# Kernel optimization log

Measured on AMD Instinct MI355X. Metric: run time of the kernel, lower is better.

Reference implementation:

```python
import jax, jax.numpy as jnp
import numpy as np

ALPHA = 0.2          # LeakyReLU negative slope
NEG_INF = -9.0e15    # padding value used by the torch code before softmax


def setup_inputs() -> dict:
    key = jax.random.key(0)
    k1, k2, k3, k4 = jax.random.split(key, 4)
    B, N, F_IN, F_OUT = 32, 1024, 128, 128
    # Dense 0/1 adjacency with self-loops (every node has degree >= 1)
    u = jax.random.uniform(k1, (B, N, N))
    adj = (u < 0.03).astype(jnp.float32)
    adj = jnp.maximum(adj, jnp.eye(N, dtype=jnp.float32)[None, :, :])
    batch_features = jax.random.normal(k2, (B, N, F_IN), dtype=jnp.float32)
    W = jax.random.normal(k3, (F_OUT, F_IN), dtype=jnp.float32) * 0.1  # nn.Linear weight [out,in]
    a = jax.random.normal(k4, (2 * F_OUT, 1), dtype=jnp.float32) * 0.1
    return {"batch_graphs": adj, "batch_features": batch_features, "W": W, "a": a}


def reference(batch_graphs, batch_features, W, a):
    # batch_graphs: [B,N,N] 0/1 adjacency; batch_features: [B,N,F_in]
    D = W.shape[0]
    h = jnp.einsum('bnf,df->bnd', batch_features, W)  # fc (no bias), dropout=0 is a no-op
    # score(i,j) = LeakyReLU(a[:D].h_i + a[D:].h_j); concat order is [center_i || neighbor_j]
    a_src = a[:D, 0]
    a_dst = a[D:, 0]
    s = h @ a_src                                   # [B,N] center term
    t = h @ a_dst                                   # [B,N] neighbor term
    scores = s[:, :, None] + t[:, None, :]          # [B,N,N]
    scores = jnp.where(scores > 0, scores, ALPHA * scores)
    # segmented softmax over each node's neighbors (pad_sequence with -9e15 == masked softmax)
    masked = jnp.where(batch_graphs == 1.0, scores, NEG_INF)
    attn = jax.nn.softmax(masked, axis=-1) * batch_graphs  # *adj zeros non-edges exactly (and deg-0 rows)
    # weighted sum of neighbor features scattered back to each node
    out = jnp.einsum('bij,bjd->bid', attn, h)       # [B,N,D]
    return out
```

## Files before the change

kernel.cpp:

```cpp
#include <hip/hip_runtime.h>
#include <hip/hip_bf16.h>

#define B_ 32
#define N_ 1024
#define F_ 128
#define ALPHA_ 0.2f
#define PSTR 72

typedef __attribute__((ext_vector_type(8))) short short8_t;
typedef __attribute__((ext_vector_type(4))) short short4_t;
typedef __attribute__((ext_vector_type(4))) float f32x4;

static __device__ __forceinline__ unsigned short bf16b(float f) {
    return __bfloat16_as_ushort(__float2bfloat16(f));
}

__global__ __launch_bounds__(256) void hst_kernel(
    const float* __restrict__ feat, const float* __restrict__ W,
    const float* __restrict__ a, float* __restrict__ h,
    float* __restrict__ s_out, float* __restrict__ t_out)
{
    __shared__ unsigned short Wt[128 * 128];
    __shared__ float fl[64 * 128];
    const int tid = threadIdx.x;
    const long row0 = (long)blockIdx.x * 64;

    for (int i = tid; i < 128 * 128; i += 256) {
        int d = i >> 7, k = i & 127;
        Wt[k * 128 + d] = bf16b(W[i]);
    }
    for (int i = tid; i < 64 * 128; i += 256) {
        int r = i >> 7, k = i & 127;
        fl[r * 128 + ((k + 8 * (r >> 2)) & 127)] = feat[(row0 + r) * 128 + k];
    }
    __syncthreads();

    const int oct = tid & 15;
    const int rg  = tid >> 4;
    const int d0  = oct * 8;
    const int r0  = rg * 4;

    float acc[4][8];
    #pragma unroll
    for (int q = 0; q < 4; ++q)
        #pragma unroll
        for (int c = 0; c < 8; ++c) acc[q][c] = 0.f;

    for (int kc = 0; kc < 128; kc += 4) {
        float wv[4][8];
        #pragma unroll
        for (int kk = 0; kk < 4; ++kk) {
            short8_t wr = *reinterpret_cast<const short8_t*>(&Wt[(kc + kk) * 128 + d0]);
            #pragma unroll
            for (int c = 0; c < 8; ++c) {
                union { unsigned u; float f; } cv;
                cv.u = ((unsigned)(unsigned short)wr[c]) << 16;
                wv[kk][c] = cv.f;
            }
        }
        #pragma unroll
        for (int q = 0; q < 4; ++q) {
            int r = r0 + q;
            int koff = (kc + 8 * (r >> 2)) & 127;
            float4 fv = *reinterpret_cast<const float4*>(&fl[r * 128 + koff]);
            float fq[4] = {fv.x, fv.y, fv.z, fv.w};
            #pragma unroll
            for (int kk = 0; kk < 4; ++kk)
                #pragma unroll
                for (int c = 0; c < 8; ++c)
                    acc[q][c] = fmaf(fq[kk], wv[kk][c], acc[q][c]);
        }
    }

    float asrc[8], adst[8];
    #pragma unroll
    for (int c = 0; c < 8; ++c) { asrc[c] = a[d0 + c]; adst[c] = a[128 + d0 + c]; }

    #pragma unroll
    for (int q = 0; q < 4; ++q) {
        long row = row0 + r0 + q;
        float4 h0 = make_float4(acc[q][0], acc[q][1], acc[q][2], acc[q][3]);
        float4 h1 = make_float4(acc[q][4], acc[q][5], acc[q][6], acc[q][7]);
        *reinterpret_cast<float4*>(&h[row * 128 + d0])     = h0;
        *reinterpret_cast<float4*>(&h[row * 128 + d0 + 4]) = h1;
        float sv = 0.f, tv = 0.f;
        #pragma unroll
        for (int c = 0; c < 8; ++c) {
            sv = fmaf(acc[q][c], asrc[c], sv);
            tv = fmaf(acc[q][c], adst[c], tv);
        }
        #pragma unroll
        for (int off = 1; off < 16; off <<= 1) {
            sv += __shfl_xor(sv, off);
            tv += __shfl_xor(tv, off);
        }
        if (oct == 0) { s_out[row] = sv; t_out[row] = tv; }
    }
}

__global__ __launch_bounds__(256) void tr_kernel(
    const float* __restrict__ h, unsigned short* __restrict__ hT)
{
    __shared__ unsigned short lt[128 * PSTR];
    const int tid = threadIdx.x;
    const int b   = blockIdx.x >> 4;
    const int j0  = (blockIdx.x & 15) * 64;

    const int j  = tid >> 2;
    const int dc = (tid & 3) * 4;
    const float* hr = h + ((size_t)(b * N_ + j0 + j)) * F_;
    #pragma unroll
    for (int q = 0; q < 8; ++q) {
        float4 v = *reinterpret_cast<const float4*>(hr + dc + q * 16);
        #pragma unroll
        for (int e = 0; e < 4; ++e)
            lt[(dc + q * 16 + e) * PSTR + j] = bf16b((&v.x)[e]);
    }
    __syncthreads();

    const int d    = tid >> 1;
    const int half = tid & 1;
    unsigned short* dst = hT + ((size_t)b * F_ + d) * N_ + j0 + half * 32;
    #pragma unroll
    for (int q = 0; q < 4; ++q)
        *reinterpret_cast<short8_t*>(dst + q * 8) =
            *reinterpret_cast<const short8_t*>(&lt[d * PSTR + half * 32 + q * 8]);
}

__global__ __launch_bounds__(512) void attn2_kernel(
    const float* __restrict__ adj, const unsigned short* __restrict__ hT,
    const float* __restrict__ s_in, const float* __restrict__ t_in,
    float* __restrict__ out)
{
    __shared__ unsigned short ht[2][128 * PSTR];
    __shared__ unsigned short pt[2][128 * PSTR];
    __shared__ float tl[N_];
    __shared__ float sl[128];
    __shared__ float rsl[128];

    const int tid = threadIdx.x;
    const int b   = blockIdx.x >> 3;
    const int i0  = (blockIdx.x & 7) * 128;

    tl[tid]       = t_in[b * N_ + tid];
    tl[tid + 512] = t_in[b * N_ + tid + 512];
    if (tid < 128) sl[tid] = s_in[b * N_ + i0 + tid];

    const int gi = tid >> 2;
    const int gj = (tid & 3) * 16;
    const float* arow = adj + ((size_t)(b * N_ + i0 + gi)) * N_;

    const unsigned short* hTb = hT + (size_t)b * F_ * N_;

    float4   a_reg[4];
    short8_t h_reg[2];
    {
        #pragma unroll
        for (int w = 0; w < 4; ++w)
            a_reg[w] = *reinterpret_cast<const float4*>(arow + gj + w * 4);
        #pragma unroll
        for (int c = 0; c < 2; ++c) {
            int ch = tid + c * 512;
            h_reg[c] = *reinterpret_cast<const short8_t*>(
                hTb + (size_t)(ch >> 3) * N_ + ((ch & 7) * 8));
        }
    }
    __syncthreads();
    const float s_i = sl[gi];

    const int w  = tid >> 6;
    const int m0 = (w >> 2) * 64;
    const int n0 = (w & 3) * 32;
    const int lm = tid & 15;
    const int kg = (tid & 63) >> 4;

    f32x4 acc[2][4];
    #pragma unroll
    for (int nf = 0; nf < 2; ++nf)
        #pragma unroll
        for (int mf = 0; mf < 4; ++mf) acc[nf][mf] = (f32x4){0.f, 0.f, 0.f, 0.f};

    float rs = 0.f;

    for (int k = 0; k < 16; ++k) {
        const int cur = k & 1;
        #pragma unroll
        for (int c = 0; c < 2; ++c) {
            int ch = tid + c * 512;
            *reinterpret_cast<short8_t*>(&ht[cur][(ch >> 3) * PSTR + (ch & 7) * 8]) = h_reg[c];
        }
        #pragma unroll
        for (int wq = 0; wq < 4; ++wq) {
            float4 t4 = *reinterpret_cast<const float4*>(&tl[k * 64 + gj + wq * 4]);
            short4_t pk;
            #pragma unroll
            for (int e = 0; e < 4; ++e) {
                float sc = s_i + (&t4.x)[e];
                sc = fmaxf(sc, ALPHA_ * sc);
                float p = __expf(sc) * (&a_reg[wq].x)[e];
                rs += p;
                pk[e] = (short)bf16b(p);
            }
            *reinterpret_cast<short4_t*>(&pt[cur][gi * PSTR + gj + wq * 4]) = pk;
        }
        if (k < 15) {
            #pragma unroll
            for (int wq = 0; wq < 4; ++wq)
                a_reg[wq] = *reinterpret_cast<const float4*>(
                    arow + (k + 1) * 64 + gj + wq * 4);
            #pragma unroll
            for (int c = 0; c < 2; ++c) {
                int ch = tid + c * 512;
                h_reg[c] = *reinterpret_cast<const short8_t*>(
                    hTb + (size_t)(ch >> 3) * N_ + ((k + 1) * 64 + (ch & 7) * 8));
            }
        }
        __syncthreads();
        #pragma unroll
        for (int ks = 0; ks < 2; ++ks) {
            short8_t bfr[2];
            #pragma unroll
            for (int nf = 0; nf < 2; ++nf)
                bfr[nf] = *reinterpret_cast<const short8_t*>(
                    &ht[cur][(n0 + nf * 16 + lm) * PSTR + ks * 32 + kg * 8]);
            #pragma unroll
            for (int mf = 0; mf < 4; ++mf) {
                short8_t afr = *reinterpret_cast<const short8_t*>(
                    &pt[cur][(m0 + mf * 16 + lm) * PSTR + ks * 32 + kg * 8]);
                acc[0][mf] = __builtin_amdgcn_mfma_f32_16x16x32_bf16(
                    afr, bfr[0], acc[0][mf], 0, 0, 0);
                acc[1][mf] = __builtin_amdgcn_mfma_f32_16x16x32_bf16(
                    afr, bfr[1], acc[1][mf], 0, 0, 0);
            }
        }
    }

    rs += __shfl_xor(rs, 1);
    rs += __shfl_xor(rs, 2);
    if ((tid & 3) == 0) rsl[gi] = 1.0f / rs;
    __syncthreads();

    const int rbase = m0 + ((tid & 63) >> 4) * 4;
    float* ob = out + ((size_t)(b * N_ + i0)) * F_;
    #pragma unroll
    for (int mf = 0; mf < 4; ++mf) {
        f32x4 inv = *reinterpret_cast<const f32x4*>(&rsl[rbase + mf * 16]);
        #pragma unroll
        for (int r = 0; r < 4; ++r) {
            int row = rbase + mf * 16 + r;
            #pragma unroll
            for (int nf = 0; nf < 2; ++nf)
                ob[(size_t)row * F_ + n0 + nf * 16 + lm] = acc[nf][mf][r] * inv[r];
        }
    }
}

extern "C" void kernel_launch(void* const* d_in, const int* in_sizes, int n_in,
                              void* d_out, int out_size, void* d_ws, size_t ws_size,
                              hipStream_t stream)
{
    const float* adj  = (const float*)d_in[0];
    const float* feat = (const float*)d_in[1];
    const float* W    = (const float*)d_in[2];
    const float* a    = (const float*)d_in[3];
    float* out = (float*)d_out;

    float* h = (float*)d_out;
    unsigned short* hT = (unsigned short*)d_ws;
    float* s = (float*)((char*)d_ws + (size_t)B_ * F_ * N_ * 2);
    float* t = s + (size_t)B_ * N_;

    hst_kernel<<<(B_ * N_) / 64, 256, 0, stream>>>(feat, W, a, h, s, t);
    tr_kernel<<<B_ * 16, 256, 0, stream>>>(h, hT);
    attn2_kernel<<<B_ * 8, 512, 0, stream>>>(adj, hT, s, t, out);
}
```

Before: 75.81 us.

## Bitpack adjacency in a separate pass and halve attention row tile

Adds a bitpack kernel that turns the fp32 adjacency into a 1-bit mask, so the attention kernel reads bytes instead of floats for the mask. The attention kernel now handles 64 rows per block instead of 128, which doubles the grid to 512 blocks, and its launch bounds ask for 4 blocks per CU. The bitpack pass still reads the full 128MB adjacency once and adds a launch plus a write of the bit array. Each h tile is now loaded twice as often per batch, and there is extra reduction work.

```diff
diff --git a/kernel.cpp b/kernel.cpp
--- a/kernel.cpp
+++ b/kernel.cpp
@@ -127,58 +127,75 @@
             *reinterpret_cast<const short8_t*>(&lt[d * PSTR + half * 32 + q * 8]);
 }
 
-__global__ __launch_bounds__(512) void attn2_kernel(
-    const float* __restrict__ adj, const unsigned short* __restrict__ hT,
+__global__ __launch_bounds__(256) void bitpack_kernel(
+    const float* __restrict__ adj, unsigned char* __restrict__ bits)
+{
+    const size_t nbytes = (size_t)B_ * N_ * N_ / 8;
+    size_t i = (size_t)blockIdx.x * 256 + threadIdx.x;
+    const size_t stride = (size_t)gridDim.x * 256;
+    for (; i < nbytes; i += stride) {
+        const float4* p = reinterpret_cast<const float4*>(adj + i * 8);
+        float4 v0 = p[0];
+        float4 v1 = p[1];
+        unsigned m = 0;
+        m |= (v0.x == 1.0f) ? 1u   : 0u;
+        m |= (v0.y == 1.0f) ? 2u   : 0u;
+        m |= (v0.z == 1.0f) ? 4u   : 0u;
+        m |= (v0.w == 1.0f) ? 8u   : 0u;
+        m |= (v1.x == 1.0f) ? 16u  : 0u;
+        m |= (v1.y == 1.0f) ? 32u  : 0u;
+        m |= (v1.z == 1.0f) ? 64u  : 0u;
+        m |= (v1.w == 1.0f) ? 128u : 0u;
+        bits[i] = (unsigned char)m;
+    }
+}
+
+__global__ __launch_bounds__(512, 4) void attn3_kernel(
+    const unsigned char* __restrict__ bits, const unsigned short* __restrict__ hT,
     const float* __restrict__ s_in, const float* __restrict__ t_in,
     float* __restrict__ out)
 {
     __shared__ unsigned short ht[2][128 * PSTR];
-    __shared__ unsigned short pt[2][128 * PSTR];
+    __shared__ unsigned short pt[2][64 * PSTR];
     __shared__ float tl[N_];
-    __shared__ float sl[128];
-    __shared__ float rsl[128];
+    __shared__ float sl[64];
+    __shared__ float rsl[64];
 
     const int tid = threadIdx.x;
-    const int b   = blockIdx.x >> 3;
-    const int i0  = (blockIdx.x & 7) * 128;
+    const int b   = blockIdx.x >> 4;
+    const int i0  = (blockIdx.x & 15) * 64;
 
     tl[tid]       = t_in[b * N_ + tid];
     tl[tid + 512] = t_in[b * N_ + tid + 512];
-    if (tid < 128) sl[tid] = s_in[b * N_ + i0 + tid];
-
-    const int gi = tid >> 2;
-    const int gj = (tid & 3) * 16;
-    const float* arow = adj + ((size_t)(b * N_ + i0 + gi)) * N_;
+    if (tid < 64) sl[tid] = s_in[b * N_ + i0 + tid];
+
+    const int gi = tid >> 3;
+    const int gj = (tid & 7) * 8;
+    const unsigned char* brow = bits + ((size_t)(b * N_ + i0 + gi)) * (N_ / 8);
 
     const unsigned short* hTb = hT + (size_t)b * F_ * N_;
 
-    float4   a_reg[4];
     short8_t h_reg[2];
-    {
-        #pragma unroll
-        for (int w = 0; w < 4; ++w)
-            a_reg[w] = *reinterpret_cast<const float4*>(arow + gj + w * 4);
-        #pragma unroll
-        for (int c = 0; c < 2; ++c) {
-            int ch = tid + c * 512;
-            h_reg[c] = *reinterpret_cast<const short8_t*>(
-                hTb + (size_t)(ch >> 3) * N_ + ((ch & 7) * 8));
-        }
+    #pragma unroll
+    for (int c = 0; c < 2; ++c) {
+        int ch = tid + c * 512;
+        h_reg[c] = *reinterpret_cast<const short8_t*>(
+            hTb + (size_t)(ch >> 3) * N_ + ((ch & 7) * 8));
     }
     __syncthreads();
     const float s_i = sl[gi];
 
     const int w  = tid >> 6;
-    const int m0 = (w >> 2) * 64;
+    const int m0 = (w >> 2) * 32;
     const int n0 = (w & 3) * 32;
     const int lm = tid & 15;
     const int kg = (tid & 63) >> 4;
 
-    f32x4 acc[2][4];
+    f32x4 acc[2][2];
     #pragma unroll
     for (int nf = 0; nf < 2; ++nf)
         #pragma unroll
-        for (int mf = 0; mf < 4; ++mf) acc[nf][mf] = (f32x4){0.f, 0.f, 0.f, 0.f};
+        for (int mf = 0; mf < 2; ++mf) acc[nf][mf] = (f32x4){0.f, 0.f, 0.f, 0.f};
 
     float rs = 0.f;
 
@@ -189,25 +206,31 @@
             int ch = tid + c * 512;
             *reinterpret_cast<short8_t*>(&ht[cur][(ch >> 3) * PSTR + (ch & 7) * 8]) = h_reg[c];
         }
-        #pragma unroll
-        for (int wq = 0; wq < 4; ++wq) {
-            float4 t4 = *reinterpret_cast<const float4*>(&tl[k * 64 + gj + wq * 4]);
-            short4_t pk;
+        {
+            unsigned bm = brow[k * 8 + (tid & 7)];
+            float4 t40 = *reinterpret_cast<const float4*>(&tl[k * 64 + gj]);
+            float4 t41 = *reinterpret_cast<const float4*>(&tl[k * 64 + gj + 4]);
+            short4_t pk0, pk1;
             #pragma unroll
             for (int e = 0; e < 4; ++e) {
-                float sc = s_i + (&t4.x)[e];
+                float sc = s_i + (&t40.x)[e];
                 sc = fmaxf(sc, ALPHA_ * sc);
-                float p = __expf(sc) * (&a_reg[wq].x)[e];
+                float p = __expf(sc) * (float)((bm >> e) & 1u);
                 rs += p;
-                pk[e] = (short)bf16b(p);
-            }
-            *reinterpret_cast<short4_t*>(&pt[cur][gi * PSTR + gj + wq * 4]) = pk;
+                pk0[e] = (short)bf16b(p);
+            }
+            #pragma unroll
+            for (int e = 0; e < 4; ++e) {
+                float sc = s_i + (&t41.x)[e];
+                sc = fmaxf(sc, ALPHA_ * sc);
+                float p = __expf(sc) * (float)((bm >> (e + 4)) & 1u);
+                rs += p;
+                pk1[e] = (short)bf16b(p);
+            }
+            *reinterpret_cast<short4_t*>(&pt[cur][gi * PSTR + gj])     = pk0;
+            *reinterpret_cast<short4_t*>(&pt[cur][gi * PSTR + gj + 4]) = pk1;
         }
         if (k < 15) {
-            #pragma unroll
-            for (int wq = 0; wq < 4; ++wq)
-                a_reg[wq] = *reinterpret_cast<const float4*>(
-                    arow + (k + 1) * 64 + gj + wq * 4);
             #pragma unroll
             for (int c = 0; c < 2; ++c) {
                 int ch = tid + c * 512;
@@ -224,7 +247,7 @@
                 bfr[nf] = *reinterpret_cast<const short8_t*>(
                     &ht[cur][(n0 + nf * 16 + lm) * PSTR + ks * 32 + kg * 8]);
             #pragma unroll
-            for (int mf = 0; mf < 4; ++mf) {
+            for (int mf = 0; mf < 2; ++mf) {
                 short8_t afr = *reinterpret_cast<const short8_t*>(
                     &pt[cur][(m0 + mf * 16 + lm) * PSTR + ks * 32 + kg * 8]);
                 acc[0][mf] = __builtin_amdgcn_mfma_f32_16x16x32_bf16(
@@ -237,13 +260,14 @@
 
     rs += __shfl_xor(rs, 1);
     rs += __shfl_xor(rs, 2);
-    if ((tid & 3) == 0) rsl[gi] = 1.0f / rs;
+    rs += __shfl_xor(rs, 4);
+    if ((tid & 7) == 0) rsl[gi] = 1.0f / rs;
     __syncthreads();
 
     const int rbase = m0 + ((tid & 63) >> 4) * 4;
     float* ob = out + ((size_t)(b * N_ + i0)) * F_;
     #pragma unroll
-    for (int mf = 0; mf < 4; ++mf) {
+    for (int mf = 0; mf < 2; ++mf) {
         f32x4 inv = *reinterpret_cast<const f32x4*>(&rsl[rbase + mf * 16]);
         #pragma unroll
         for (int r = 0; r < 4; ++r) {
@@ -269,8 +293,10 @@
     unsigned short* hT = (unsigned short*)d_ws;
     float* s = (float*)((char*)d_ws + (size_t)B_ * F_ * N_ * 2);
     float* t = s + (size_t)B_ * N_;
+    unsigned char* bits = (unsigned char*)(t + (size_t)B_ * N_);
 
     hst_kernel<<<(B_ * N_) / 64, 256, 0, stream>>>(feat, W, a, h, s, t);
     tr_kernel<<<B_ * 16, 256, 0, stream>>>(h, hT);
-    attn2_kernel<<<B_ * 8, 512, 0, stream>>>(adj, hT, s, t, out);
-}
+    bitpack_kernel<<<2048, 256, 0, stream>>>(adj, bits);
+    attn3_kernel<<<B_ * 16, 512, 0, stream>>>(bits, hT, s, t, out);
+}
```

Result: slower. 86.95 us (+14.7%).
